# Kernel optimization log

Measured on AMD Instinct MI355X. Metric: run time of the kernel, lower is better.

## Reference

```python
import jax, jax.numpy as jnp
import numpy as np

DIM = 1024
HEADS = 16
HEAD_DIM = DIM // HEADS
SCALE = HEAD_DIM ** -0.5


def setup_inputs() -> dict:
    key = jax.random.key(0)
    k1, k2, k3, k4 = jax.random.split(key, 4)
    x = jax.random.normal(k1, (2, 2048, DIM), dtype=jnp.float32)
    # nn.Linear(dim, 3*dim, bias=False): weight shape (3*dim, dim), y = x @ W.T
    w_qkv = jax.random.normal(k2, (3 * DIM, DIM), dtype=jnp.float32) * (DIM ** -0.5)
    w_proj = jax.random.normal(k3, (DIM, DIM), dtype=jnp.float32) * (DIM ** -0.5)
    head_w = jnp.ones((HEADS,), dtype=jnp.float32)
    return {"x": x, "w_qkv": w_qkv, "w_proj": w_proj, "head_w": head_w}


def reference(x, w_qkv, w_proj, head_w) -> jnp.ndarray:
    B, N, C = x.shape
    qkv = jnp.einsum("bnc,dc->bnd", x, w_qkv)  # [B,N,3C]
    qkv = qkv.reshape(B, N, 3, HEADS, HEAD_DIM).transpose(2, 0, 3, 1, 4)
    q, k, v = qkv[0], qkv[1], qkv[2]  # each [B,H,N,Dh]
    attn = jnp.einsum("bhqd,bhkd->bhqk", q, k) * SCALE  # [B,H,N,N]
    attn = jax.nn.softmax(attn, axis=-1)
    out = jnp.einsum("bhqk,bhkd->bhqd", attn, v)  # [B,H,N,Dh]
    hw = jax.nn.softmax(head_w)[None, :, None, None]
    out = out * hw
    out = out.transpose(0, 2, 1, 3).reshape(B, N, C)
    return jnp.einsum("bnc,dc->bnd", out, w_proj)
```

## Files before the change

### kernel.cpp

```cpp
#include <hip/hip_runtime.h>

typedef _Float16 half_t;
typedef _Float16 half8 __attribute__((ext_vector_type(8)));
typedef _Float16 half4_t __attribute__((ext_vector_type(4)));
typedef float floatx4 __attribute__((ext_vector_type(4)));
typedef float floatx16 __attribute__((ext_vector_type(16)));

#define B_SZ 2
#define SEQ 2048
#define DIM_ 1024
#define NH 16
#define DH 64
#define ROWS (B_SZ * SEQ)

__device__ __forceinline__ void gl2lds16(const void* g, void* l) {
  __builtin_amdgcn_global_load_lds((const __attribute__((address_space(1))) unsigned int*)g,
                                   (__attribute__((address_space(3))) unsigned int*)l, 16, 0, 0);
}

__global__ __launch_bounds__(256) void convert_all(const float4* __restrict__ x,
                                                   const float4* __restrict__ wq,
                                                   const float4* __restrict__ wp,
                                                   half4_t* __restrict__ dst,
                                                   int nx, int nq, int np) {
  int i = blockIdx.x * blockDim.x + threadIdx.x;
  float4 v;
  if (i < nx) v = x[i];
  else if (i < nx + nq) v = wq[i - nx];
  else if (i < nx + nq + np) v = wp[i - nx - nq];
  else return;
  half4_t h;
  h.x = (half_t)v.x; h.y = (half_t)v.y; h.z = (half_t)v.z; h.w = (half_t)v.w;
  dst[i] = h;
}

template <int MODE, int BN>
__global__ __launch_bounds__(256, 3) void gemm32(const half_t* __restrict__ A,
                                                 const half_t* __restrict__ Bt,
                                                 half_t* __restrict__ q16,
                                                 half_t* __restrict__ k16,
                                                 half_t* __restrict__ vT16,
                                                 float* __restrict__ outp) {
  constexpr int K = 1024;
  constexpr int BK = 32;
  constexpr int NT = BN / 64;
  __shared__ __align__(16) half_t a_lds[2][128 * BK];
  __shared__ __align__(16) half_t b_lds[2][BN * BK];
  const int t = threadIdx.x;
  const int wave = t >> 6, lane = t & 63;
  const int l31 = lane & 31, hw = lane >> 5;
  const int wm = wave >> 1, wn = wave & 1;
  const int row0 = blockIdx.y * 128, col0 = blockIdx.x * BN;

  floatx16 acc[2][NT];
#pragma unroll
  for (int i = 0; i < 2; ++i)
#pragma unroll
    for (int j = 0; j < NT; ++j)
#pragma unroll
      for (int r = 0; r < 16; ++r) acc[i][j][r] = 0.f;

  auto stage = [&](int buf, int k0) {
#pragma unroll
    for (int hi = 0; hi < 2; ++hi) {
      int s = t + hi * 256;
      int row = s >> 2, c = s & 3;
      int sc = c ^ ((row >> 1) & 3);
      gl2lds16(A + (size_t)(row0 + row) * K + (k0 + sc * 8),
               &a_lds[buf][(wave * 64 + hi * 256) * 8]);
    }
#pragma unroll
    for (int hi = 0; hi < BN / 64; ++hi) {
      int s = t + hi * 256;
      int row = s >> 2, c = s & 3;
      int sc = c ^ ((row >> 1) & 3);
      gl2lds16(Bt + (size_t)(col0 + row) * K + (k0 + sc * 8),
               &b_lds[buf][(wave * 64 + hi * 256) * 8]);
    }
  };

  stage(0, 0);
  int cur = 0;
  for (int k0 = 0; k0 < K; k0 += BK) {
    __syncthreads();
    if (k0 + BK < K) stage(cur ^ 1, k0 + BK);

#pragma unroll
    for (int kf = 0; kf < 2; ++kf) {
      half8 af[2], bf[NT];
#pragma unroll
      for (int mt = 0; mt < 2; ++mt) {
        int row = wm * 64 + mt * 32 + l31;
        af[mt] = *(const half8*)(&a_lds[cur][row * BK + (((kf << 1) | hw) ^ ((row >> 1) & 3)) * 8]);
      }
#pragma unroll
      for (int nt = 0; nt < NT; ++nt) {
        int row = wn * (BN / 2) + nt * 32 + l31;
        bf[nt] = *(const half8*)(&b_lds[cur][row * BK + (((kf << 1) | hw) ^ ((row >> 1) & 3)) * 8]);
      }
#pragma unroll
      for (int mt = 0; mt < 2; ++mt)
#pragma unroll
        for (int nt = 0; nt < NT; ++nt)
          acc[mt][nt] = __builtin_amdgcn_mfma_f32_32x32x16_f16(af[mt], bf[nt], acc[mt][nt], 0, 0, 0);
    }
    cur ^= 1;
  }

  if (MODE == 0) {
    const int which = col0 >> 10;
#pragma unroll
    for (int mt = 0; mt < 2; ++mt)
#pragma unroll
      for (int nt = 0; nt < NT; ++nt) {
        int growb = row0 + wm * 64 + mt * 32;
        int gcol = col0 + wn * (BN / 2) + nt * 32 + l31;
        int hc = gcol & 1023, h = hc >> 6, d = hc & 63;
        if (which == 2) {
#pragma unroll
          for (int rq = 0; rq < 4; ++rq) {
            int grow = growb + 8 * rq + 4 * hw;
            int b = grow >> 11, n0 = grow & 2047;
            int bh = b * NH + h;
            half4_t h4;
            h4.x = (half_t)acc[mt][nt][rq * 4 + 0];
            h4.y = (half_t)acc[mt][nt][rq * 4 + 1];
            h4.z = (half_t)acc[mt][nt][rq * 4 + 2];
            h4.w = (half_t)acc[mt][nt][rq * 4 + 3];
            *(half4_t*)(vT16 + ((size_t)bh * DH + d) * SEQ + n0) = h4;
          }
        } else {
#pragma unroll
          for (int r = 0; r < 16; ++r) {
            int grow = growb + (r & 3) + 8 * (r >> 2) + 4 * hw;
            int b = grow >> 11, n = grow & 2047;
            int bh = b * NH + h;
            float v = acc[mt][nt][r];
            if (which == 0)
              q16[((size_t)bh * SEQ + n) * DH + d] = (half_t)(v * 0.125f);
            else
              k16[((size_t)bh * SEQ + n) * DH + d] = (half_t)v;
          }
        }
      }
  } else {
#pragma unroll
    for (int mt = 0; mt < 2; ++mt)
#pragma unroll
      for (int nt = 0; nt < NT; ++nt) {
        int growb = row0 + wm * 64 + mt * 32;
        int gcol = col0 + wn * (BN / 2) + nt * 32 + l31;
#pragma unroll
        for (int r = 0; r < 16; ++r) {
          int grow = growb + (r & 3) + 8 * (r >> 2) + 4 * hw;
          outp[(size_t)grow * DIM_ + gcol] = acc[mt][nt][r];
        }
      }
  }
}

__global__ __launch_bounds__(256, 4) void attn_p1(const half_t* __restrict__ q16,
                                                  const half_t* __restrict__ k16,
                                                  const half_t* __restrict__ vT16,
                                                  half_t* __restrict__ opart,
                                                  float* __restrict__ psums) {
  __shared__ __align__(16) half_t k_lds[2][64 * 64];
  __shared__ __align__(16) half_t v_lds[2][64 * 64];

  const int t = threadIdx.x;
  const int wave = t >> 6, lane = t & 63;
  const int l15 = lane & 15, quad = lane >> 4;
  const int blk = blockIdx.x;
  const int js = blk & 1, qt = (blk >> 1) & 15, bh = blk >> 5;
  const half_t* qp = q16 + (size_t)bh * SEQ * DH;
  const half_t* kp = k16 + (size_t)bh * SEQ * DH;
  const half_t* vp = vT16 + (size_t)bh * DH * SEQ;
  const int q0w = qt * 128 + wave * 32;
  const int jbase = js * 1024;

  const int s0 = t, s1 = t + 256;
  const int r0_ = s0 >> 3, c0_ = (s0 & 7) ^ (r0_ & 7);
  const int r1_ = s1 >> 3, c1_ = (s1 & 7) ^ (r1_ & 7);

  half8 qf[2][2];
#pragma unroll
  for (int mi = 0; mi < 2; ++mi)
#pragma unroll
    for (int kf = 0; kf < 2; ++kf)
      qf[mi][kf] = *(const half8*)(qp + (size_t)(q0w + mi * 16 + l15) * DH + kf * 32 + quad * 8);

  const floatx4 z4 = {0.f, 0.f, 0.f, 0.f};
  floatx4 o[2][4];
  float psum[2] = {0.f, 0.f};
#pragma unroll
  for (int mi = 0; mi < 2; ++mi)
#pragma unroll
    for (int i = 0; i < 4; ++i) o[mi][i] = z4;

  gl2lds16(kp + (size_t)(jbase + r0_) * DH + c0_ * 8, &k_lds[0][(wave * 64) * 8]);
  gl2lds16(vp + (size_t)r0_ * SEQ + jbase + c0_ * 8, &v_lds[0][(wave * 64) * 8]);
  gl2lds16(kp + (size_t)(jbase + r1_) * DH + c1_ * 8, &k_lds[0][(wave * 64 + 256) * 8]);
  gl2lds16(vp + (size_t)r1_ * SEQ + jbase + c1_ * 8, &v_lds[0][(wave * 64 + 256) * 8]);

  int cur = 0;
  for (int jt = 0; jt < 16; ++jt) {
    __syncthreads();

    if (jt + 1 < 16) {
      const int j0 = jbase + (jt + 1) * 64, nb = cur ^ 1;
      gl2lds16(kp + (size_t)(j0 + r0_) * DH + c0_ * 8, &k_lds[nb][(wave * 64) * 8]);
      gl2lds16(vp + (size_t)r0_ * SEQ + j0 + c0_ * 8, &v_lds[nb][(wave * 64) * 8]);
      gl2lds16(kp + (size_t)(j0 + r1_) * DH + c1_ * 8, &k_lds[nb][(wave * 64 + 256) * 8]);
      gl2lds16(vp + (size_t)r1_ * SEQ + j0 + c1_ * 8, &v_lds[nb][(wave * 64 + 256) * 8]);
    }

    const half_t* kl = k_lds[cur];
    const half_t* vl = v_lds[cur];

    half4_t pf[2][4];
#pragma unroll
    for (int nt = 0; nt < 4; ++nt) {
      int row = nt * 16 + l15;
      floatx4 st0 = z4, st1 = z4;
#pragma unroll
      for (int kf = 0; kf < 2; ++kf) {
        half8 kb = *(const half8*)(kl + row * 64 + (((kf << 2) | quad) ^ (row & 7)) * 8);
        st0 = __builtin_amdgcn_mfma_f32_16x16x32_f16(kb, qf[0][kf], st0, 0, 0, 0);
        st1 = __builtin_amdgcn_mfma_f32_16x16x32_f16(kb, qf[1][kf], st1, 0, 0, 0);
      }
      {
        float p0 = __expf(st0[0]), p1 = __expf(st0[1]);
        float p2 = __expf(st0[2]), p3 = __expf(st0[3]);
        psum[0] += (p0 + p1) + (p2 + p3);
        half4_t pk;
        pk.x = (half_t)p0; pk.y = (half_t)p1; pk.z = (half_t)p2; pk.w = (half_t)p3;
        pf[0][nt] = pk;
      }
      {
        float p0 = __expf(st1[0]), p1 = __expf(st1[1]);
        float p2 = __expf(st1[2]), p3 = __expf(st1[3]);
        psum[1] += (p0 + p1) + (p2 + p3);
        half4_t pk;
        pk.x = (half_t)p0; pk.y = (half_t)p1; pk.z = (half_t)p2; pk.w = (half_t)p3;
        pf[1][nt] = pk;
      }
    }

#pragma unroll
    for (int jt2 = 0; jt2 < 4; ++jt2)
#pragma unroll
      for (int dt = 0; dt < 4; ++dt) {
        int row = dt * 16 + l15;
        int ch = (jt2 * 2 + (quad >> 1)) ^ (l15 & 7);
        half4_t vb = *(const half4_t*)(vl + row * 64 + ch * 8 + (quad & 1) * 4);
        o[0][dt] = __builtin_amdgcn_mfma_f32_16x16x16f16(pf[0][jt2], vb, o[0][dt], 0, 0, 0);
        o[1][dt] = __builtin_amdgcn_mfma_f32_16x16x16f16(pf[1][jt2], vb, o[1][dt], 0, 0, 0);
      }
    cur ^= 1;
  }

#pragma unroll
  for (int mi = 0; mi < 2; ++mi) {
    psum[mi] += __shfl_xor(psum[mi], 16, 64);
    psum[mi] += __shfl_xor(psum[mi], 32, 64);
  }
  if (quad == 0) {
#pragma unroll
    for (int mi = 0; mi < 2; ++mi)
      psums[((size_t)(js * 32 + bh)) * SEQ + q0w + mi * 16 + l15] = psum[mi];
  }

#pragma unroll
  for (int mi = 0; mi < 2; ++mi)
#pragma unroll
    for (int r = 0; r < 4; ++r) {
      int n = q0w + mi * 16 + quad * 4 + r;
      size_t base = ((size_t)(js * 32 + bh) * SEQ + n) * DH;
#pragma unroll
      for (int dt = 0; dt < 4; ++dt)
        opart[base + dt * 16 + l15] = (half_t)o[mi][dt][r];
    }
}

__global__ __launch_bounds__(256) void combine(const half_t* __restrict__ opart,
                                               const float* __restrict__ psums,
                                               const float* __restrict__ head_w,
                                               half_t* __restrict__ attn16) {
  int idx = blockIdx.x * blockDim.x + threadIdx.x;
  int d4 = idx & 15, n = (idx >> 4) & 2047, bh = idx >> 15;
  int h = bh & 15, b = bh >> 4;
  const size_t jstr = (size_t)32 * SEQ * DH;
  size_t off = ((size_t)bh * SEQ + n) * DH + d4 * 4;
  half4_t o0 = *(const half4_t*)(opart + off);
  half4_t o1 = *(const half4_t*)(opart + jstr + off);
  float ps = psums[(size_t)bh * SEQ + n] + psums[(size_t)32 * SEQ + (size_t)bh * SEQ + n];

  float mw = head_w[0];
#pragma unroll
  for (int i = 1; i < NH; ++i) mw = fmaxf(mw, head_w[i]);
  float sw = 0.f;
#pragma unroll
  for (int i = 0; i < NH; ++i) sw += __expf(head_w[i] - mw);
  float hwv = __expf(head_w[h] - mw) / sw;

  float scl = hwv / ps;
  half4_t r;
  r.x = (half_t)(((float)o0.x + (float)o1.x) * scl);
  r.y = (half_t)(((float)o0.y + (float)o1.y) * scl);
  r.z = (half_t)(((float)o0.z + (float)o1.z) * scl);
  r.w = (half_t)(((float)o0.w + (float)o1.w) * scl);
  *(half4_t*)(attn16 + ((size_t)(b * SEQ + n)) * DIM_ + h * DH + d4 * 4) = r;
}

extern "C" void kernel_launch(void* const* d_in, const int* in_sizes, int n_in,
                              void* d_out, int out_size, void* d_ws, size_t ws_size,
                              hipStream_t stream) {
  const float* x = (const float*)d_in[0];
  const float* w_qkv = (const float*)d_in[1];
  const float* w_proj = (const float*)d_in[2];
  const float* head_w = (const float*)d_in[3];
  float* out = (float*)d_out;

  half_t* x16 = (half_t*)d_ws;
  half_t* wq16 = x16 + (size_t)ROWS * DIM_;
  half_t* wp16 = wq16 + (size_t)3 * DIM_ * DIM_;
  half_t* q16 = wp16 + (size_t)DIM_ * DIM_;
  half_t* k16 = q16 + (size_t)ROWS * DIM_;
  half_t* vT16 = k16 + (size_t)ROWS * DIM_;
  half_t* attn16 = vT16 + (size_t)ROWS * DIM_;
  half_t* opart = attn16 + (size_t)ROWS * DIM_;
  float* psums = (float*)(opart + (size_t)2 * 32 * SEQ * DH);

  const int nx = ROWS * DIM_ / 4, nq = 3 * DIM_ * DIM_ / 4, np = DIM_ * DIM_ / 4;
  convert_all<<<(nx + nq + np) / 256, 256, 0, stream>>>((const float4*)x, (const float4*)w_qkv,
                                                        (const float4*)w_proj, (half4_t*)x16,
                                                        nx, nq, np);

  gemm32<0, 128><<<dim3(24, 32), 256, 0, stream>>>(x16, wq16, q16, k16, vT16, nullptr);
  attn_p1<<<32 * 16 * 2, 256, 0, stream>>>(q16, k16, vT16, opart, psums);
  combine<<<(32 * SEQ * DH / 4) / 256, 256, 0, stream>>>(opart, psums, head_w, attn16);
  gemm32<1, 64><<<dim3(16, 32), 256, 0, stream>>>(attn16, wp16, nullptr, nullptr, nullptr, out);
}
```

Baseline: 198.5 us.

## Use exp2 with folded log2e scale, MFMA row sums, and pair-row LDS layout

Folds log2(e) into the Q scaling so the softmax can use the raw hardware exp2 instruction instead of __expf. Row sums of P are now computed by an extra MFMA against a vector of ones, replacing the scalar adds and cross-lane shuffles. The GEMM staging also changes its LDS layout to interleave pairs of rows per 64-element chunk with a new XOR swizzle, aimed at reducing bank conflicts. The row sums now come from the fp16-rounded probabilities, which adds MFMA work and slightly changes numerics.

```diff
diff --git a/kernel.cpp b/kernel.cpp
--- a/kernel.cpp
+++ b/kernel.cpp
@@ -64,16 +64,18 @@
 #pragma unroll
     for (int hi = 0; hi < 2; ++hi) {
       int s = t + hi * 256;
-      int row = s >> 2, c = s & 3;
-      int sc = c ^ ((row >> 1) & 3);
+      int row = ((s >> 3) << 1) | (s & 1);
+      int c = (s >> 1) & 3;
+      int sc = c ^ ((row >> 2) & 3);
       gl2lds16(A + (size_t)(row0 + row) * K + (k0 + sc * 8),
                &a_lds[buf][(wave * 64 + hi * 256) * 8]);
     }
 #pragma unroll
     for (int hi = 0; hi < BN / 64; ++hi) {
       int s = t + hi * 256;
-      int row = s >> 2, c = s & 3;
-      int sc = c ^ ((row >> 1) & 3);
+      int row = ((s >> 3) << 1) | (s & 1);
+      int c = (s >> 1) & 3;
+      int sc = c ^ ((row >> 2) & 3);
       gl2lds16(Bt + (size_t)(col0 + row) * K + (k0 + sc * 8),
                &b_lds[buf][(wave * 64 + hi * 256) * 8]);
     }
@@ -91,12 +93,14 @@
 #pragma unroll
       for (int mt = 0; mt < 2; ++mt) {
         int row = wm * 64 + mt * 32 + l31;
-        af[mt] = *(const half8*)(&a_lds[cur][row * BK + (((kf << 1) | hw) ^ ((row >> 1) & 3)) * 8]);
+        int c_lds = ((kf << 1) | hw) ^ ((row >> 2) & 3);
+        af[mt] = *(const half8*)(&a_lds[cur][(row >> 1) * 64 + c_lds * 16 + (row & 1) * 8]);
       }
 #pragma unroll
       for (int nt = 0; nt < NT; ++nt) {
         int row = wn * (BN / 2) + nt * 32 + l31;
-        bf[nt] = *(const half8*)(&b_lds[cur][row * BK + (((kf << 1) | hw) ^ ((row >> 1) & 3)) * 8]);
+        int c_lds = ((kf << 1) | hw) ^ ((row >> 2) & 3);
+        bf[nt] = *(const half8*)(&b_lds[cur][(row >> 1) * 64 + c_lds * 16 + (row & 1) * 8]);
       }
 #pragma unroll
       for (int mt = 0; mt < 2; ++mt)
@@ -137,7 +141,7 @@
             int bh = b * NH + h;
             float v = acc[mt][nt][r];
             if (which == 0)
-              q16[((size_t)bh * SEQ + n) * DH + d] = (half_t)(v * 0.125f);
+              q16[((size_t)bh * SEQ + n) * DH + d] = (half_t)(v * 0.18033688011112042f);
             else
               k16[((size_t)bh * SEQ + n) * DH + d] = (half_t)v;
           }
@@ -191,16 +195,21 @@
 
   const floatx4 z4 = {0.f, 0.f, 0.f, 0.f};
   floatx4 o[2][4];
-  float psum[2] = {0.f, 0.f};
-#pragma unroll
-  for (int mi = 0; mi < 2; ++mi)
+  floatx4 osum[2];
+#pragma unroll
+  for (int mi = 0; mi < 2; ++mi) {
+    osum[mi] = z4;
 #pragma unroll
     for (int i = 0; i < 4; ++i) o[mi][i] = z4;
+  }
 
   gl2lds16(kp + (size_t)(jbase + r0_) * DH + c0_ * 8, &k_lds[0][(wave * 64) * 8]);
   gl2lds16(vp + (size_t)r0_ * SEQ + jbase + c0_ * 8, &v_lds[0][(wave * 64) * 8]);
   gl2lds16(kp + (size_t)(jbase + r1_) * DH + c1_ * 8, &k_lds[0][(wave * 64 + 256) * 8]);
   gl2lds16(vp + (size_t)r1_ * SEQ + jbase + c1_ * 8, &v_lds[0][(wave * 64 + 256) * 8]);
+
+  const half_t one_h = (half_t)1.f;
+  const half4_t vone = {one_h, one_h, one_h, one_h};
 
   int cur = 0;
   for (int jt = 0; jt < 16; ++jt) {
@@ -229,25 +238,25 @@
         st1 = __builtin_amdgcn_mfma_f32_16x16x32_f16(kb, qf[1][kf], st1, 0, 0, 0);
       }
       {
-        float p0 = __expf(st0[0]), p1 = __expf(st0[1]);
-        float p2 = __expf(st0[2]), p3 = __expf(st0[3]);
-        psum[0] += (p0 + p1) + (p2 + p3);
         half4_t pk;
-        pk.x = (half_t)p0; pk.y = (half_t)p1; pk.z = (half_t)p2; pk.w = (half_t)p3;
+        pk.x = (half_t)__builtin_amdgcn_exp2f(st0[0]);
+        pk.y = (half_t)__builtin_amdgcn_exp2f(st0[1]);
+        pk.z = (half_t)__builtin_amdgcn_exp2f(st0[2]);
+        pk.w = (half_t)__builtin_amdgcn_exp2f(st0[3]);
         pf[0][nt] = pk;
       }
       {
-        float p0 = __expf(st1[0]), p1 = __expf(st1[1]);
-        float p2 = __expf(st1[2]), p3 = __expf(st1[3]);
-        psum[1] += (p0 + p1) + (p2 + p3);
         half4_t pk;
-        pk.x = (half_t)p0; pk.y = (half_t)p1; pk.z = (half_t)p2; pk.w = (half_t)p3;
+        pk.x = (half_t)__builtin_amdgcn_exp2f(st1[0]);
+        pk.y = (half_t)__builtin_amdgcn_exp2f(st1[1]);
+        pk.z = (half_t)__builtin_amdgcn_exp2f(st1[2]);
+        pk.w = (half_t)__builtin_amdgcn_exp2f(st1[3]);
         pf[1][nt] = pk;
       }
     }
 
 #pragma unroll
-    for (int jt2 = 0; jt2 < 4; ++jt2)
+    for (int jt2 = 0; jt2 < 4; ++jt2) {
 #pragma unroll
       for (int dt = 0; dt < 4; ++dt) {
         int row = dt * 16 + l15;
@@ -256,18 +265,18 @@
         o[0][dt] = __builtin_amdgcn_mfma_f32_16x16x16f16(pf[0][jt2], vb, o[0][dt], 0, 0, 0);
         o[1][dt] = __builtin_amdgcn_mfma_f32_16x16x16f16(pf[1][jt2], vb, o[1][dt], 0, 0, 0);
       }
+      osum[0] = __builtin_amdgcn_mfma_f32_16x16x16f16(pf[0][jt2], vone, osum[0], 0, 0, 0);
+      osum[1] = __builtin_amdgcn_mfma_f32_16x16x16f16(pf[1][jt2], vone, osum[1], 0, 0, 0);
+    }
     cur ^= 1;
   }
 
-#pragma unroll
-  for (int mi = 0; mi < 2; ++mi) {
-    psum[mi] += __shfl_xor(psum[mi], 16, 64);
-    psum[mi] += __shfl_xor(psum[mi], 32, 64);
-  }
-  if (quad == 0) {
+  if (l15 == 0) {
 #pragma unroll
     for (int mi = 0; mi < 2; ++mi)
-      psums[((size_t)(js * 32 + bh)) * SEQ + q0w + mi * 16 + l15] = psum[mi];
+#pragma unroll
+      for (int r = 0; r < 4; ++r)
+        psums[((size_t)(js * 32 + bh)) * SEQ + q0w + mi * 16 + quad * 4 + r] = osum[mi][r];
   }
 
 #pragma unroll
```

Result: no change. 200.6 us (+1.0%).
